# Kernel tuning notes

Measured on AMD Instinct MI355X. Metric: run time of the kernel, lower is better.

Reference implementation:

```python
import jax, jax.numpy as jnp
import numpy as np

B, N, C, H, REG = 1, 2309, 1024, 16, 5
D = C // H


def setup_inputs() -> dict:
    key = jax.random.key(0)
    k0, k1, k2, k3 = jax.random.split(key, 4)
    x = jax.random.normal(k0, (B, N, C), dtype=jnp.float32)
    g_info = jax.random.normal(k1, (12, 2, C), dtype=jnp.float32)
    W_qkv = jax.random.normal(k2, (C, 3 * C), dtype=jnp.float32) * 0.02
    W_proj = jax.random.normal(k3, (C, C), dtype=jnp.float32) * 0.02
    b_proj = jnp.zeros((C,), dtype=jnp.float32)
    return {"x": x, "g_info": g_info, "W_qkv": W_qkv, "W_proj": W_proj, "b_proj": b_proj}


def reference(x, g_info, W_qkv, W_proj, b_proj):
    Bx, Nx, Cx = x.shape
    scale = D ** -0.5
    # qkv projection (qkv_bias=False)
    qkv = (x @ W_qkv).reshape(Bx, Nx, 3, H, D)
    q, k, v = qkv[:, :, 0], qkv[:, :, 1], qkv[:, :, 2]  # [B,N,H,D]

    # grounding query vector from layer 0
    g_layer = g_info[0].reshape(-1, H, D)
    q_g = g_layer[0]  # [H,D]

    # cosine-similarity routing over non-register tokens
    q_pure = q[:, REG:]  # [B,M,H,D]
    q_n = q_pure / jnp.linalg.norm(q_pure, axis=-1, keepdims=True)
    qg_n = q_g / jnp.linalg.norm(q_g, axis=-1, keepdims=True)
    sim = (qg_n[None, None] * q_n).sum(-1).mean(-1)  # [B,M]
    sim = (sim - sim.min()) / (sim.max() - sim.min())  # global min-max normalize
    pos = sim > 0.9  # [B,M] boolean routing mask

    # Full logits computed once; group attention = masked softmax over the
    # group's key set (registers always included). This is mathematically
    # identical to the torch gather->attend->scatter, with static shapes.
    logits = jnp.einsum('bqhd,bkhd->bhqk', q * scale, k)  # [B,H,N,N]

    def masked_attn(tok_mask):
        key_mask = jnp.concatenate([jnp.ones((Bx, REG), bool), tok_mask], axis=1)  # [B,N]
        l = jnp.where(key_mask[:, None, None, :], logits, -jnp.inf)
        a = jax.nn.softmax(l, axis=-1)
        return jnp.einsum('bhqk,bkhd->bqhd', a, v)  # [B,N,H,D]

    x_pos = masked_attn(pos)
    x_neg = masked_attn(~pos)

    reg_out = (x_pos[:, :REG] + x_neg[:, :REG]) * 0.5
    tok_out = jnp.where(pos[:, :, None, None], x_pos[:, REG:], x_neg[:, REG:])
    out = jnp.concatenate([reg_out, tok_out], axis=1).reshape(Bx, Nx, Cx)
    return out @ W_proj + b_proj
```

## Files before the change

### kernel.cpp

```cpp
#include <hip/hip_runtime.h>
#include <math.h>

#define TOK 2309
#define CH 1024
#define NH 16
#define HD 64
#define NREG 5
#define NTOK (TOK - NREG)
#define NPADQ 2432
#define NPAD2 2432
#define NKT 38
#define HTILES 19
#define NQROW 2368
#define QSCL 0.1803368801f

typedef unsigned short ushort_t;
typedef unsigned char uchar_t;
typedef __attribute__((ext_vector_type(8))) short s8frag;
typedef __attribute__((ext_vector_type(4))) float f4frag;
typedef __attribute__((ext_vector_type(2))) long ll2;

__device__ __forceinline__ unsigned short f2bf(float x){
  union { float f; unsigned u; } v; v.f = x;
  unsigned r = v.u + 0x7FFF + ((v.u >> 16) & 1);
  return (unsigned short)(r >> 16);
}
__device__ __forceinline__ float bf2f(unsigned short u){
  union { unsigned u32; float f; } v; v.u32 = ((unsigned)u) << 16;
  return v.f;
}
__device__ __forceinline__ unsigned pack_bf16(float lo, float hi){
  union { float f; unsigned u; } a, b;
  a.f = lo; b.f = hi;
  return __builtin_amdgcn_perm(b.u + 0x8000u, a.u + 0x8000u, 0x07060302u);
}
__device__ __forceinline__ uchar_t f2fp8(float x){
  return (uchar_t)(__builtin_amdgcn_cvt_pk_fp8_f32(x, x, 0, false) & 0xff);
}
__device__ __forceinline__ void cp16(const void* g, void* l){
  __builtin_amdgcn_global_load_lds(
      (const __attribute__((address_space(1))) unsigned int*)g,
      (__attribute__((address_space(3))) unsigned int*)l, 16, 0, 0);
}

__global__ __launch_bounds__(256) void split_x_kernel(
    const float* __restrict__ X, ushort_t* __restrict__ Xbf)
{
  int row = blockIdx.x;
  int c4 = threadIdx.x * 4;
  ushort4 h4 = {0,0,0,0};
  if (row < TOK) {
    float4 v = *(const float4*)&X[(size_t)row*CH + c4];
    h4.x = f2bf(v.x); h4.y = f2bf(v.y); h4.z = f2bf(v.z); h4.w = f2bf(v.w);
  }
  *(ushort4*)&Xbf[(size_t)row*CH + c4] = h4;
}

__global__ __launch_bounds__(256) void pack_w_kernel(
    const float* __restrict__ Wqkv, const float* __restrict__ Wproj,
    ushort_t* __restrict__ WqkvT, ushort_t* __restrict__ WprojT)
{
  __shared__ float T[64][68];
  const int tid = threadIdx.x;
  int bx = blockIdx.x;
  const float* W; ushort_t* WT; int N;
  if (bx < 48) { W = Wqkv; WT = WqkvT; N = 3*CH; }
  else         { W = Wproj; WT = WprojT; N = CH; bx -= 48; }
  const int n0 = bx * 64;
  const int k0 = blockIdx.y * 64;
  const int lr = tid >> 4;
  const int lc = (tid & 15) * 4;
  #pragma unroll
  for (int s = 0; s < 4; s++) {
    float4 v = *(const float4*)&W[(size_t)(k0 + lr + s*16) * N + n0 + lc];
    *(float4*)&T[lr + s*16][lc] = v;
  }
  __syncthreads();
  const int nl = tid >> 2;
  const int kc = (tid & 3) * 16;
  ushort_t* dh = WT + (size_t)(n0 + nl) * CH + k0 + kc;
  #pragma unroll
  for (int g = 0; g < 4; g++) {
    ushort4 oh;
    oh.x = f2bf(T[kc+g*4+0][nl]); oh.y = f2bf(T[kc+g*4+1][nl]);
    oh.z = f2bf(T[kc+g*4+2][nl]); oh.w = f2bf(T[kc+g*4+3][nl]);
    *(ushort4*)&dh[g*4] = oh;
  }
}

__global__ __launch_bounds__(256) void ghat_kernel(
    const float* __restrict__ G, const float* __restrict__ Wqkv,
    float* __restrict__ U)
{
  const int tid = threadIdx.x;
  const int k = blockIdx.x * 16 + (tid >> 4);
  const int h = tid & 15;
  const float* g = G + h*64;
  float n2 = 0.f;
  #pragma unroll
  for (int d = 0; d < 64; d += 4) {
    float4 gv = *(const float4*)&g[d];
    n2 += gv.x*gv.x + gv.y*gv.y + gv.z*gv.z + gv.w*gv.w;
  }
  const float inv = 1.f / sqrtf(n2);
  const float* wr = Wqkv + (size_t)k*(3*CH) + h*64;
  float dot = 0.f;
  #pragma unroll
  for (int d = 0; d < 64; d += 4) {
    float4 wv = *(const float4*)&wr[d];
    float4 gv = *(const float4*)&g[d];
    dot += wv.x*gv.x + wv.y*gv.y + wv.z*gv.z + wv.w*gv.w;
  }
  U[h*CH + k] = dot * inv;
}

__global__ __launch_bounds__(256) void gemm_qkv_mfma(
    const ushort_t* __restrict__ Xbf, const ushort_t* __restrict__ WT,
    ushort_t* __restrict__ Qbf, uchar_t* __restrict__ Q8,
    uchar_t* __restrict__ K8, ushort_t* __restrict__ Vbf)
{
  __shared__ ushort_t LA[2][4096];
  __shared__ ushort_t LB[2][4096];
  const int tid = threadIdx.x;
  const int w = tid >> 6, lane = tid & 63;
  const int quad = lane >> 4, c16 = lane & 15;
  const int wm = w >> 1, wn = w & 1;
  const int nt = blockIdx.x, mt = blockIdx.y;
  const int n0 = nt * 128, m0 = mt * 128;

  const int srow = tid >> 2;
  const int g = (tid & 3) ^ ((tid >> 3) & 3);
  const size_t aoff = (size_t)(m0 + srow)*CH + g*8;
  const size_t boff = (size_t)(n0 + srow)*CH + g*8;
  const int lbase = (tid & 192) * 8;

  f4frag acc[4][4];
  #pragma unroll
  for (int mi = 0; mi < 4; mi++)
    #pragma unroll
    for (int nb = 0; nb < 4; nb++) acc[mi][nb] = (f4frag){0.f,0.f,0.f,0.f};

  const int soff = (quad ^ ((c16 >> 1) & 3)) * 8;
  int aro[4], bro[4];
  #pragma unroll
  for (int i = 0; i < 4; i++) {
    aro[i] = (wm*64 + i*16 + c16)*32 + soff;
    bro[i] = (wn*64 + i*16 + c16)*32 + soff;
  }

#define QKV_STAGE(KT, BUF) {                                                   \
    const int _k = (KT)*32;                                                    \
    cp16(Xbf + aoff + _k,                 &LA[BUF][lbase]);                    \
    cp16(Xbf + aoff + _k + (size_t)64*CH, &LA[BUF][2048 + lbase]);             \
    cp16(WT  + boff + _k,                 &LB[BUF][lbase]);                    \
    cp16(WT  + boff + _k + (size_t)64*CH, &LB[BUF][2048 + lbase]);             \
    }

  QKV_STAGE(0, 0);
  for (int kt = 0; kt < 32; kt++) {
    const int buf = kt & 1;
    __syncthreads();
    if (kt < 31) { QKV_STAGE(kt+1, buf^1); }
    s8frag a[4], b[4];
    #pragma unroll
    for (int i = 0; i < 4; i++) a[i] = *(const s8frag*)&LA[buf][aro[i]];
    #pragma unroll
    for (int i = 0; i < 4; i++) b[i] = *(const s8frag*)&LB[buf][bro[i]];
    #pragma unroll
    for (int mi = 0; mi < 4; mi++)
      #pragma unroll
      for (int nb = 0; nb < 4; nb++)
        acc[mi][nb] = __builtin_amdgcn_mfma_f32_16x16x32_bf16(a[mi], b[nb], acc[mi][nb], 0, 0, 0);
  }
#undef QKV_STAGE

  const int three = (nt >= 16) ? 2 : (nt >= 8) ? 1 : 0;
  #pragma unroll
  for (int mi = 0; mi < 4; mi++) {
    const int orow = m0 + wm*64 + mi*16 + quad*4;
    if (three == 0) {
      #pragma unroll
      for (int nb = 0; nb < 4; nb++) {
        const int col = n0 + wn*64 + nb*16 + c16;
        const int h = (col >> 6) & 15, d = col & 63;
        ushort_t* qb = Qbf + (size_t)h*NPADQ*64;
        uchar_t*  q8 = Q8 + (size_t)h*NPADQ*64;
        #pragma unroll
        for (int r = 0; r < 4; r++) {
          int row = orow + r;
          float v = (row < TOK) ? acc[mi][nb][r] : 0.f;
          qb[(size_t)row*64 + d] = f2bf(v);
          q8[(size_t)row*64 + d] = f2fp8(v);
        }
      }
    } else if (three == 1) {
      #pragma unroll
      for (int nb = 0; nb < 4; nb++) {
        const int col = n0 + wn*64 + nb*16 + c16;
        const int h = (col >> 6) & 15;
        const int quadK = ((nb & 1) * 2) + (c16 >> 3);
        const int byteoff = (nb >> 1) * 8 + (c16 & 7);
        uchar_t* base = K8 + (size_t)h*NKT*4096;
        #pragma unroll
        for (int r = 0; r < 4; r++) {
          int row = orow + r;
          float v = (row < TOK) ? acc[mi][nb][r] * QSCL : 0.f;
          int tile = row >> 6, b = (row >> 4) & 3, c16K = row & 15;
          base[(size_t)tile*4096 + b*1024 + (quadK*16 + c16K)*16 + byteoff] = f2fp8(v);
        }
      }
    } else {
      const int tile  = orow >> 6;
      const int jj    = orow & 63;
      const int c     = jj >> 5;
      const int t16   = (jj >> 4) & 1;
      const int quadA = (jj >> 2) & 3;
      #pragma unroll
      for (int nb = 0; nb < 4; nb++) {
        const int col = n0 + wn*64 + nb*16 + c16;
        const int h = (col >> 6) & 15, d = col & 63;
        const int dblk = d >> 4, c16A = d & 15;
        ushort_t* base = Vbf + (size_t)h*NKT*4096;
        ushort4 o;
        o.x = f2bf((orow+0 < TOK) ? acc[mi][nb][0] : 0.f);
        o.y = f2bf((orow+1 < TOK) ? acc[mi][nb][1] : 0.f);
        o.z = f2bf((orow+2 < TOK) ? acc[mi][nb][2] : 0.f);
        o.w = f2bf((orow+3 < TOK) ? acc[mi][nb][3] : 0.f);
        *(ushort4*)&base[(size_t)tile*4096 + dblk*1024 + c*512
                         + (quadA*16 + c16A)*8 + 4*t16] = o;
      }
    }
  }
}

__global__ __launch_bounds__(256) void sim_kernel(
    const float* __restrict__ X, const float* __restrict__ U,
    const ushort_t* __restrict__ Qbf, float* __restrict__ sim)
{
  const int gid = blockIdx.x*256 + threadIdx.x;
  const int it = gid >> 4;
  const int h  = gid & 15;
  const int row = NREG + it;
  const float* xr = X + (size_t)row*CH;
  const float* ur = U + h*CH;
  float num = 0.f;
  for (int k = 0; k < CH; k += 4) {
    float4 xv = *(const float4*)&xr[k];
    float4 uv = *(const float4*)&ur[k];
    num += xv.x*uv.x + xv.y*uv.y + xv.z*uv.z + xv.w*uv.w;
  }
  const ushort_t* qr = Qbf + ((size_t)h*NPADQ + row)*64;
  float n2 = 0.f;
  #pragma unroll
  for (int d = 0; d < 64; d += 4) {
    ushort4 a = *(const ushort4*)&qr[d];
    float q0 = bf2f(a.x), q1 = bf2f(a.y), q2 = bf2f(a.z), q3 = bf2f(a.w);
    n2 += q0*q0 + q1*q1 + q2*q2 + q3*q3;
  }
  float acc = num / sqrtf(n2);
  acc += __shfl_xor(acc, 1, 64);
  acc += __shfl_xor(acc, 2, 64);
  acc += __shfl_xor(acc, 4, 64);
  acc += __shfl_xor(acc, 8, 64);
  if (h == 0) sim[it] = acc * (1.0f/16.0f);
}

__global__ __launch_bounds__(256) void mask_kernel(
    const float* __restrict__ sim, int* __restrict__ cls,
    float* __restrict__ WP, float* __restrict__ WN)
{
  __shared__ float smn[256], smx[256];
  const int tid = threadIdx.x;
  float mn = 1e30f, mx = -1e30f;
  for (int i = tid; i < NTOK; i += 256) { float s = sim[i]; mn = fminf(mn, s); mx = fmaxf(mx, s); }
  smn[tid] = mn; smx[tid] = mx;
  __syncthreads();
  for (int off = 128; off > 0; off >>= 1) {
    if (tid < off) { smn[tid] = fminf(smn[tid], smn[tid+off]); smx[tid] = fmaxf(smx[tid], smx[tid+off]); }
    __syncthreads();
  }
  mn = smn[0]; mx = smx[0];
  float inv = 1.0f / (mx - mn);
  for (int j = tid; j < NPAD2; j += 256) {
    float wp = 0.f, wn = 0.f; int c = 0;
    if (j < NREG) { wp = 1.f; wn = 1.f; c = 2; }
    else if (j < TOK) {
      bool pos = ((sim[j-NREG] - mn) * inv) > 0.9f;
      c = pos ? 1 : 0;
      wp = pos ? 1.f : 0.f;
      wn = pos ? 0.f : 1.f;
    }
    WP[j] = wp; WN[j] = wn;
    if (j < TOK) cls[j] = c;
  }
}

__global__ __launch_bounds__(256) void attn_kernel(
    const uchar_t* __restrict__ Q8, const uchar_t* __restrict__ K8,
    const ushort_t* __restrict__ Vbf,
    const float* __restrict__ WP, const float* __restrict__ WN,
    ushort_t* __restrict__ POp, ushort_t* __restrict__ POn,
    float* __restrict__ Lp, float* __restrict__ Ln)
{
  __shared__ __align__(16) uchar_t smem[24576];
  uchar_t* Kst = smem;
  uchar_t* Vst = smem + 8192;
  const int tid = threadIdx.x;
  const int w = tid >> 6, lane = tid & 63;
  const int quad = lane >> 4, c16 = lane & 15;
  const int h = blockIdx.y;
  const int half = blockIdx.z;
  const int q0 = blockIdx.x * 64;

  const uchar_t* Qh = Q8 + (size_t)h * NPADQ * 64;
  const uchar_t* gk = K8 + ((size_t)h*NKT + half*HTILES)*4096 + tid*16;
  const uchar_t* gv = (const uchar_t*)Vbf + ((size_t)h*NKT + half*HTILES)*8192 + tid*16;
  const int lw = w * 1024;

  const uchar_t* qp = Qh + (size_t)(q0 + w*16 + c16)*64 + quad*8;
  const long qf0 = *(const long*)(qp);
  const long qf1 = *(const long*)(qp + 32);

  f4frag op[4], on[4];
  #pragma unroll
  for (int nb = 0; nb < 4; nb++) { op[nb] = (f4frag){0.f,0.f,0.f,0.f}; on[nb] = (f4frag){0.f,0.f,0.f,0.f}; }
  float lp = 0.f, ln = 0.f;

  cp16(gk, Kst + lw);
  cp16(gv, Vst + lw);
  cp16(gv + 4096, Vst + 4096 + lw);

  int pb = 0;
  for (int t = 0; t < HTILES; t++) {
    __syncthreads();
    if (t < HTILES-1) {
      cp16(gk + (size_t)(t+1)*4096, Kst + (pb^1)*4096 + lw);
      cp16(gv + (size_t)(t+1)*8192,        Vst + (pb^1)*8192 + lw);
      cp16(gv + (size_t)(t+1)*8192 + 4096, Vst + (pb^1)*8192 + 4096 + lw);
    }
    const int j0 = half*(HTILES*64) + t*64;
    f4frag st[4];
    #pragma unroll
    for (int b = 0; b < 4; b++) {
      ll2 kv = *(const ll2*)&Kst[pb*4096 + b*1024 + lane*16];
      f4frag z = (f4frag){0.f,0.f,0.f,0.f};
      z     = __builtin_amdgcn_mfma_f32_16x16x32_fp8_fp8(kv.x, qf0, z, 0, 0, 0);
      st[b] = __builtin_amdgcn_mfma_f32_16x16x32_fp8_fp8(kv.y, qf1, z, 0, 0, 0);
    }
    unsigned pu[4][2], nu[4][2];
    #pragma unroll
    for (int b = 0; b < 4; b++) {
      float4 wp4 = *(const float4*)&WP[j0 + b*16 + quad*4];
      float4 wn4 = *(const float4*)&WN[j0 + b*16 + quad*4];
      float p0 = __builtin_amdgcn_exp2f(st[b][0]);
      float p1 = __builtin_amdgcn_exp2f(st[b][1]);
      float p2 = __builtin_amdgcn_exp2f(st[b][2]);
      float p3 = __builtin_amdgcn_exp2f(st[b][3]);
      float a0 = p0*wp4.x, a1 = p1*wp4.y, a2 = p2*wp4.z, a3 = p3*wp4.w;
      float b0 = p0*wn4.x, b1 = p1*wn4.y, b2 = p2*wn4.z, b3 = p3*wn4.w;
      lp += (a0+a1)+(a2+a3);
      ln += (b0+b1)+(b2+b3);
      pu[b][0] = pack_bf16(a0, a1); pu[b][1] = pack_bf16(a2, a3);
      nu[b][0] = pack_bf16(b0, b1); nu[b][1] = pack_bf16(b2, b3);
    }
    union Frag { unsigned u[4]; s8frag v; };
    Frag fp0, fp1, fn0, fn1;
    fp0.u[0]=pu[0][0]; fp0.u[1]=pu[0][1]; fp0.u[2]=pu[1][0]; fp0.u[3]=pu[1][1];
    fp1.u[0]=pu[2][0]; fp1.u[1]=pu[2][1]; fp1.u[2]=pu[3][0]; fp1.u[3]=pu[3][1];
    fn0.u[0]=nu[0][0]; fn0.u[1]=nu[0][1]; fn0.u[2]=nu[1][0]; fn0.u[3]=nu[1][1];
    fn1.u[0]=nu[2][0]; fn1.u[1]=nu[2][1]; fn1.u[2]=nu[3][0]; fn1.u[3]=nu[3][1];
    #pragma unroll
    for (int nb = 0; nb < 4; nb++) {
      s8frag va = *(const s8frag*)&Vst[pb*8192 + nb*2048 + lane*16];
      s8frag vb = *(const s8frag*)&Vst[pb*8192 + nb*2048 + 1024 + lane*16];
      op[nb] = __builtin_amdgcn_mfma_f32_16x16x32_bf16(va, fp0.v, op[nb], 0, 0, 0);
      op[nb] = __builtin_amdgcn_mfma_f32_16x16x32_bf16(vb, fp1.v, op[nb], 0, 0, 0);
      on[nb] = __builtin_amdgcn_mfma_f32_16x16x32_bf16(va, fn0.v, on[nb], 0, 0, 0);
      on[nb] = __builtin_amdgcn_mfma_f32_16x16x32_bf16(vb, fn1.v, on[nb], 0, 0, 0);
    }
    pb ^= 1;
  }

  lp += __shfl_xor(lp, 16, 64); lp += __shfl_xor(lp, 32, 64);
  ln += __shfl_xor(ln, 16, 64); ln += __shfl_xor(ln, 32, 64);
  const int iq = q0 + w*16 + c16;
  if (quad == 0 && iq < TOK) {
    Lp[((size_t)half*NH + h)*NQROW + iq] = lp;
    Ln[((size_t)half*NH + h)*NQROW + iq] = ln;
  }
  if (iq < TOK) {
    const size_t base = (size_t)half*NQROW*CH + (size_t)iq*CH + h*HD;
    #pragma unroll
    for (int nb = 0; nb < 4; nb++) {
      uint2 po, no;
      po.x = pack_bf16(op[nb][0], op[nb][1]);
      po.y = pack_bf16(op[nb][2], op[nb][3]);
      no.x = pack_bf16(on[nb][0], on[nb][1]);
      no.y = pack_bf16(on[nb][2], on[nb][3]);
      *(uint2*)(POp + base + nb*16 + quad*4) = po;
      *(uint2*)(POn + base + nb*16 + quad*4) = no;
    }
  }
}

__global__ __launch_bounds__(256) void merge_kernel(
    const ushort_t* __restrict__ POp, const ushort_t* __restrict__ POn,
    const float* __restrict__ Lp, const float* __restrict__ Ln,
    const int* __restrict__ cls, ushort_t* __restrict__ AObf)
{
  const int row = blockIdx.x;
  const int c4 = threadIdx.x * 4;
  const int h = c4 >> 6;
  const size_t o0 = (size_t)row*CH + c4;
  const size_t o1 = (size_t)NQROW*CH + o0;
  ushort4 p0 = *(const ushort4*)(POp + o0);
  ushort4 p1 = *(const ushort4*)(POp + o1);
  ushort4 n0 = *(const ushort4*)(POn + o0);
  ushort4 n1 = *(const ushort4*)(POn + o1);
  const float lpt = Lp[(size_t)h*NQROW + row] + Lp[(size_t)(NH+h)*NQROW + row];
  const float lnt = Ln[(size_t)h*NQROW + row] + Ln[(size_t)(NH+h)*NQROW + row];
  const float ilp = 1.f / lpt, iln = 1.f / lnt;
  const int cq = cls[row];
  float vp[4], vn[4], o[4];
  vp[0] = (bf2f(p0.x)+bf2f(p1.x))*ilp; vn[0] = (bf2f(n0.x)+bf2f(n1.x))*iln;
  vp[1] = (bf2f(p0.y)+bf2f(p1.y))*ilp; vn[1] = (bf2f(n0.y)+bf2f(n1.y))*iln;
  vp[2] = (bf2f(p0.z)+bf2f(p1.z))*ilp; vn[2] = (bf2f(n0.z)+bf2f(n1.z))*iln;
  vp[3] = (bf2f(p0.w)+bf2f(p1.w))*ilp; vn[3] = (bf2f(n0.w)+bf2f(n1.w))*iln;
  if (row < NREG) {
    #pragma unroll
    for (int i = 0; i < 4; i++) o[i] = 0.5f*(vp[i]+vn[i]);
  } else if (cq == 1) {
    #pragma unroll
    for (int i = 0; i < 4; i++) o[i] = vp[i];
  } else {
    #pragma unroll
    for (int i = 0; i < 4; i++) o[i] = vn[i];
  }
  uint2 pk;
  pk.x = pack_bf16(o[0], o[1]);
  pk.y = pack_bf16(o[2], o[3]);
  *(uint2*)(AObf + (size_t)row*CH + c4) = pk;
}

__global__ __launch_bounds__(256) void gemm_proj_mfma(
    const ushort_t* __restrict__ A, const ushort_t* __restrict__ WT,
    const float* __restrict__ bp, float* __restrict__ out)
{
  __shared__ ushort_t LA[2][4096];
  __shared__ ushort_t LB[2][2048];
  const int tid = threadIdx.x;
  const int w = tid >> 6, lane = tid & 63;
  const int quad = lane >> 4, c16 = lane & 15;
  const int wm = w >> 1, wn = w & 1;
  const int nt = blockIdx.x, mt = blockIdx.y;
  const int n0 = nt * 64, m0 = mt * 128;

  const int srow = tid >> 2;
  const int g = (tid & 3) ^ ((tid >> 3) & 3);
  const size_t aoff = (size_t)(m0 + srow)*CH + g*8;
  const size_t boff = (size_t)(n0 + srow)*CH + g*8;
  const int lbase = (tid & 192) * 8;

  f4frag acc[4][2];
  #pragma unroll
  for (int mi = 0; mi < 4; mi++)
    #pragma unroll
    for (int nb = 0; nb < 2; nb++) acc[mi][nb] = (f4frag){0.f,0.f,0.f,0.f};

  const int soff = (quad ^ ((c16 >> 1) & 3)) * 8;
  int aro[4], bro[2];
  #pragma unroll
  for (int i = 0; i < 4; i++) aro[i] = (wm*64 + i*16 + c16)*32 + soff;
  #pragma unroll
  for (int i = 0; i < 2; i++) bro[i] = (wn*32 + i*16 + c16)*32 + soff;

#define PROJ_STAGE(KT, BUF) {                                                  \
    const int _k = (KT)*32;                                                    \
    cp16(A  + aoff + _k,                 &LA[BUF][lbase]);                     \
    cp16(A  + aoff + _k + (size_t)64*CH, &LA[BUF][2048 + lbase]);              \
    cp16(WT + boff + _k,                 &LB[BUF][lbase]);                     \
    }

  PROJ_STAGE(0, 0);
  for (int kt = 0; kt < 32; kt++) {
    const int buf = kt & 1;
    __syncthreads();
    if (kt < 31) { PROJ_STAGE(kt+1, buf^1); }
    s8frag a[4], b[2];
    #pragma unroll
    for (int i = 0; i < 4; i++) a[i] = *(const s8frag*)&LA[buf][aro[i]];
    #pragma unroll
    for (int i = 0; i < 2; i++) b[i] = *(const s8frag*)&LB[buf][bro[i]];
    #pragma unroll
    for (int mi = 0; mi < 4; mi++)
      #pragma unroll
      for (int nb = 0; nb < 2; nb++)
        acc[mi][nb] = __builtin_amdgcn_mfma_f32_16x16x32_bf16(a[mi], b[nb], acc[mi][nb], 0, 0, 0);
  }
#undef PROJ_STAGE

  #pragma unroll
  for (int mi = 0; mi < 4; mi++) {
    const int orow = m0 + wm*64 + mi*16 + quad*4;
    #pragma unroll
    for (int nb = 0; nb < 2; nb++) {
      const int col = n0 + wn*32 + nb*16 + c16;
      const float bias = bp[col];
      #pragma unroll
      for (int r = 0; r < 4; r++) {
        int row = orow + r;
        if (row < TOK) out[(size_t)row*CH + col] = acc[mi][nb][r] + bias;
      }
    }
  }
}

extern "C" void kernel_launch(void* const* d_in, const int* in_sizes, int n_in,
                              void* d_out, int out_size, void* d_ws, size_t ws_size,
                              hipStream_t stream) {
  const float* x      = (const float*)d_in[0];
  const float* g_info = (const float*)d_in[1];
  const float* W_qkv  = (const float*)d_in[2];
  const float* W_proj = (const float*)d_in[3];
  const float* b_proj = (const float*)d_in[4];
  float* out = (float*)d_out;

  float* ws = (float*)d_ws;
  float* SIM = ws;
  float* WP  = SIM + NTOK;
  float* WN  = WP + NPAD2;
  int*   CLS = (int*)(WN + NPAD2);
  float* LpB = (float*)(CLS + 2312);
  float* LnB = LpB + (size_t)2*NH*NQROW;
  float* U   = LnB + (size_t)2*NH*NQROW;
  ushort_t* Xbf    = (ushort_t*)(U + (size_t)NH*CH);
  ushort_t* WqkvT  = Xbf    + (size_t)NPADQ*CH;
  ushort_t* WprojT = WqkvT  + (size_t)3*CH*CH;
  ushort_t* Qbf    = WprojT + (size_t)CH*CH;
  ushort_t* AObf   = Qbf    + (size_t)NH*NPADQ*64;
  ushort_t* POp    = AObf   + (size_t)NPADQ*CH;
  ushort_t* POn    = POp    + (size_t)2*NQROW*CH;
  uchar_t*  Q8     = (uchar_t*)(POn + (size_t)2*NQROW*CH);
  uchar_t*  K8     = Q8 + (size_t)NH*NPADQ*64;
  ushort_t* Vbf    = (ushort_t*)(K8 + (size_t)NH*NKT*4096);

  split_x_kernel<<<dim3(NPADQ), 256, 0, stream>>>(x, Xbf);
  pack_w_kernel<<<dim3(64, 16), 256, 0, stream>>>(W_qkv, W_proj, WqkvT, WprojT);
  ghat_kernel<<<dim3(64), 256, 0, stream>>>(g_info, W_qkv, U);
  gemm_qkv_mfma<<<dim3(24, 19), 256, 0, stream>>>(Xbf, WqkvT, Qbf, Q8, K8, Vbf);
  sim_kernel<<<dim3(144), 256, 0, stream>>>(x, U, Qbf, SIM);
  mask_kernel<<<dim3(1), 256, 0, stream>>>(SIM, CLS, WP, WN);
  attn_kernel<<<dim3(37, NH, 2), 256, 0, stream>>>(Q8, K8, Vbf, WP, WN,
                                                   POp, POn, LpB, LnB);
  merge_kernel<<<dim3(TOK), 256, 0, stream>>>(POp, POn, LpB, LnB, CLS, AObf);
  gemm_proj_mfma<<<dim3(16, 19), 256, 0, stream>>>(AObf, WprojT, b_proj, out);
}
```

Baseline: 265.0 us.

## Fuse prep kernels into one launch and parallelize sim over tokens

Merges the x bf16 conversion, weight transpose/pack and grounding-vector projection into a single prep kernel dispatched by block index, removing two kernel launches. The sim kernel is restructured so each block handles one token: x is staged in LDS, the 1024-long dot product is split across 16 segments per head against a transposed U layout, and partial sums are reduced through shared memory. This is meant to replace the old 144-block launch, where each thread looped over all 1024 channels, with much more parallelism. The cost is more blocks and extra LDS traffic and syncs.

After: 232.2 us. 1.14x faster.

```diff
diff --git a/kernel.cpp b/kernel.cpp
--- a/kernel.cpp
+++ b/kernel.cpp
@@ -43,75 +43,76 @@
       (__attribute__((address_space(3))) unsigned int*)l, 16, 0, 0);
 }
 
-__global__ __launch_bounds__(256) void split_x_kernel(
-    const float* __restrict__ X, ushort_t* __restrict__ Xbf)
-{
-  int row = blockIdx.x;
-  int c4 = threadIdx.x * 4;
-  ushort4 h4 = {0,0,0,0};
-  if (row < TOK) {
-    float4 v = *(const float4*)&X[(size_t)row*CH + c4];
-    h4.x = f2bf(v.x); h4.y = f2bf(v.y); h4.z = f2bf(v.z); h4.w = f2bf(v.w);
-  }
-  *(ushort4*)&Xbf[(size_t)row*CH + c4] = h4;
-}
-
-__global__ __launch_bounds__(256) void pack_w_kernel(
-    const float* __restrict__ Wqkv, const float* __restrict__ Wproj,
-    ushort_t* __restrict__ WqkvT, ushort_t* __restrict__ WprojT)
-{
-  __shared__ float T[64][68];
+__global__ __launch_bounds__(256) void prep_kernel(
+    const float* __restrict__ X, const float* __restrict__ Wqkv,
+    const float* __restrict__ Wproj, const float* __restrict__ G,
+    ushort_t* __restrict__ Xbf, ushort_t* __restrict__ WqkvT,
+    ushort_t* __restrict__ WprojT, float* __restrict__ UT)
+{
   const int tid = threadIdx.x;
   int bx = blockIdx.x;
-  const float* W; ushort_t* WT; int N;
-  if (bx < 48) { W = Wqkv; WT = WqkvT; N = 3*CH; }
-  else         { W = Wproj; WT = WprojT; N = CH; bx -= 48; }
-  const int n0 = bx * 64;
-  const int k0 = blockIdx.y * 64;
-  const int lr = tid >> 4;
-  const int lc = (tid & 15) * 4;
-  #pragma unroll
-  for (int s = 0; s < 4; s++) {
-    float4 v = *(const float4*)&W[(size_t)(k0 + lr + s*16) * N + n0 + lc];
-    *(float4*)&T[lr + s*16][lc] = v;
-  }
-  __syncthreads();
-  const int nl = tid >> 2;
-  const int kc = (tid & 3) * 16;
-  ushort_t* dh = WT + (size_t)(n0 + nl) * CH + k0 + kc;
-  #pragma unroll
-  for (int g = 0; g < 4; g++) {
-    ushort4 oh;
-    oh.x = f2bf(T[kc+g*4+0][nl]); oh.y = f2bf(T[kc+g*4+1][nl]);
-    oh.z = f2bf(T[kc+g*4+2][nl]); oh.w = f2bf(T[kc+g*4+3][nl]);
-    *(ushort4*)&dh[g*4] = oh;
-  }
-}
-
-__global__ __launch_bounds__(256) void ghat_kernel(
-    const float* __restrict__ G, const float* __restrict__ Wqkv,
-    float* __restrict__ U)
-{
-  const int tid = threadIdx.x;
-  const int k = blockIdx.x * 16 + (tid >> 4);
-  const int h = tid & 15;
-  const float* g = G + h*64;
-  float n2 = 0.f;
-  #pragma unroll
-  for (int d = 0; d < 64; d += 4) {
-    float4 gv = *(const float4*)&g[d];
-    n2 += gv.x*gv.x + gv.y*gv.y + gv.z*gv.z + gv.w*gv.w;
-  }
-  const float inv = 1.f / sqrtf(n2);
-  const float* wr = Wqkv + (size_t)k*(3*CH) + h*64;
-  float dot = 0.f;
-  #pragma unroll
-  for (int d = 0; d < 64; d += 4) {
-    float4 wv = *(const float4*)&wr[d];
-    float4 gv = *(const float4*)&g[d];
-    dot += wv.x*gv.x + wv.y*gv.y + wv.z*gv.z + wv.w*gv.w;
-  }
-  U[h*CH + k] = dot * inv;
+  if (bx < NPADQ) {
+    const int row = bx;
+    const int c4 = tid * 4;
+    ushort4 h4 = {0,0,0,0};
+    if (row < TOK) {
+      float4 v = *(const float4*)&X[(size_t)row*CH + c4];
+      h4.x = f2bf(v.x); h4.y = f2bf(v.y); h4.z = f2bf(v.z); h4.w = f2bf(v.w);
+    }
+    *(ushort4*)&Xbf[(size_t)row*CH + c4] = h4;
+    return;
+  }
+  bx -= NPADQ;
+  if (bx < 1024) {
+    __shared__ float T[64][68];
+    int nb_i = bx & 63;
+    const int k0 = (bx >> 6) * 64;
+    const float* W; ushort_t* WT; int N;
+    if (nb_i < 48) { W = Wqkv; WT = WqkvT; N = 3*CH; }
+    else           { W = Wproj; WT = WprojT; N = CH; nb_i -= 48; }
+    const int n0 = nb_i * 64;
+    const int lr = tid >> 4;
+    const int lc = (tid & 15) * 4;
+    #pragma unroll
+    for (int s = 0; s < 4; s++) {
+      float4 v = *(const float4*)&W[(size_t)(k0 + lr + s*16) * N + n0 + lc];
+      *(float4*)&T[lr + s*16][lc] = v;
+    }
+    __syncthreads();
+    const int nl = tid >> 2;
+    const int kc = (tid & 3) * 16;
+    ushort_t* dh = WT + (size_t)(n0 + nl) * CH + k0 + kc;
+    #pragma unroll
+    for (int g = 0; g < 4; g++) {
+      ushort4 oh;
+      oh.x = f2bf(T[kc+g*4+0][nl]); oh.y = f2bf(T[kc+g*4+1][nl]);
+      oh.z = f2bf(T[kc+g*4+2][nl]); oh.w = f2bf(T[kc+g*4+3][nl]);
+      *(ushort4*)&dh[g*4] = oh;
+    }
+    return;
+  }
+  bx -= 1024;
+  {
+    const int k = bx * 16 + (tid >> 4);
+    const int h = tid & 15;
+    const float* g = G + h*64;
+    float n2 = 0.f;
+    #pragma unroll
+    for (int d = 0; d < 64; d += 4) {
+      float4 gv = *(const float4*)&g[d];
+      n2 += gv.x*gv.x + gv.y*gv.y + gv.z*gv.z + gv.w*gv.w;
+    }
+    const float inv = 1.f / sqrtf(n2);
+    const float* wr = Wqkv + (size_t)k*(3*CH) + h*64;
+    float dot = 0.f;
+    #pragma unroll
+    for (int d = 0; d < 64; d += 4) {
+      float4 wv = *(const float4*)&wr[d];
+      float4 gv = *(const float4*)&g[d];
+      dot += wv.x*gv.x + wv.y*gv.y + wv.z*gv.z + wv.w*gv.w;
+    }
+    UT[k*16 + h] = dot * inv;
+  }
 }
 
 __global__ __launch_bounds__(256) void gemm_qkv_mfma(
@@ -234,35 +235,39 @@
 }
 
 __global__ __launch_bounds__(256) void sim_kernel(
-    const float* __restrict__ X, const float* __restrict__ U,
+    const float* __restrict__ X, const float* __restrict__ UT,
     const ushort_t* __restrict__ Qbf, float* __restrict__ sim)
 {
-  const int gid = blockIdx.x*256 + threadIdx.x;
-  const int it = gid >> 4;
-  const int h  = gid & 15;
-  const int row = NREG + it;
-  const float* xr = X + (size_t)row*CH;
-  const float* ur = U + h*CH;
+  __shared__ float xs[1024];
+  __shared__ float pnum[16][17];
+  __shared__ float pn2[16][17];
+  const int tid = threadIdx.x;
+  const int row = NREG + blockIdx.x;
+  *(float4*)&xs[tid*4] = *(const float4*)&X[(size_t)row*CH + tid*4];
+  __syncthreads();
+  const int h = tid & 15, seg = tid >> 4;
+  const int k0 = seg * 64;
   float num = 0.f;
-  for (int k = 0; k < CH; k += 4) {
-    float4 xv = *(const float4*)&xr[k];
-    float4 uv = *(const float4*)&ur[k];
-    num += xv.x*uv.x + xv.y*uv.y + xv.z*uv.z + xv.w*uv.w;
-  }
-  const ushort_t* qr = Qbf + ((size_t)h*NPADQ + row)*64;
-  float n2 = 0.f;
-  #pragma unroll
-  for (int d = 0; d < 64; d += 4) {
-    ushort4 a = *(const ushort4*)&qr[d];
-    float q0 = bf2f(a.x), q1 = bf2f(a.y), q2 = bf2f(a.z), q3 = bf2f(a.w);
-    n2 += q0*q0 + q1*q1 + q2*q2 + q3*q3;
-  }
-  float acc = num / sqrtf(n2);
-  acc += __shfl_xor(acc, 1, 64);
-  acc += __shfl_xor(acc, 2, 64);
-  acc += __shfl_xor(acc, 4, 64);
-  acc += __shfl_xor(acc, 8, 64);
-  if (h == 0) sim[it] = acc * (1.0f/16.0f);
+  #pragma unroll
+  for (int j = 0; j < 64; j++)
+    num += xs[k0 + j] * UT[(k0 + j)*16 + h];
+  const ushort_t* qr = Qbf + ((size_t)h*NPADQ + row)*64 + seg*4;
+  ushort4 a = *(const ushort4*)qr;
+  float q0 = bf2f(a.x), q1 = bf2f(a.y), q2 = bf2f(a.z), q3 = bf2f(a.w);
+  pnum[seg][h] = num;
+  pn2[seg][h] = q0*q0 + q1*q1 + q2*q2 + q3*q3;
+  __syncthreads();
+  if (tid < 16) {
+    float nsum = 0.f, dsum = 0.f;
+    #pragma unroll
+    for (int s = 0; s < 16; s++) { nsum += pnum[s][tid]; dsum += pn2[s][tid]; }
+    float acc = nsum / sqrtf(dsum);
+    acc += __shfl_xor(acc, 1, 64);
+    acc += __shfl_xor(acc, 2, 64);
+    acc += __shfl_xor(acc, 4, 64);
+    acc += __shfl_xor(acc, 8, 64);
+    if (tid == 0) sim[blockIdx.x] = acc * (1.0f/16.0f);
+  }
 }
 
 __global__ __launch_bounds__(256) void mask_kernel(
@@ -532,8 +537,8 @@
   int*   CLS = (int*)(WN + NPAD2);
   float* LpB = (float*)(CLS + 2312);
   float* LnB = LpB + (size_t)2*NH*NQROW;
-  float* U   = LnB + (size_t)2*NH*NQROW;
-  ushort_t* Xbf    = (ushort_t*)(U + (size_t)NH*CH);
+  float* UT  = LnB + (size_t)2*NH*NQROW;
+  ushort_t* Xbf    = (ushort_t*)(UT + (size_t)CH*NH);
   ushort_t* WqkvT  = Xbf    + (size_t)NPADQ*CH;
   ushort_t* WprojT = WqkvT  + (size_t)3*CH*CH;
   ushort_t* Qbf    = WprojT + (size_t)CH*CH;
@@ -544,11 +549,10 @@
   uchar_t*  K8     = Q8 + (size_t)NH*NPADQ*64;
   ushort_t* Vbf    = (ushort_t*)(K8 + (size_t)NH*NKT*4096);
 
-  split_x_kernel<<<dim3(NPADQ), 256, 0, stream>>>(x, Xbf);
-  pack_w_kernel<<<dim3(64, 16), 256, 0, stream>>>(W_qkv, W_proj, WqkvT, WprojT);
-  ghat_kernel<<<dim3(64), 256, 0, stream>>>(g_info, W_qkv, U);
+  prep_kernel<<<dim3(NPADQ + 1024 + 64), 256, 0, stream>>>(
+      x, W_qkv, W_proj, g_info, Xbf, WqkvT, WprojT, UT);
   gemm_qkv_mfma<<<dim3(24, 19), 256, 0, stream>>>(Xbf, WqkvT, Qbf, Q8, K8, Vbf);
-  sim_kernel<<<dim3(144), 256, 0, stream>>>(x, U, Qbf, SIM);
+  sim_kernel<<<dim3(NTOK), 256, 0, stream>>>(x, UT, Qbf, SIM);
   mask_kernel<<<dim3(1), 256, 0, stream>>>(SIM, CLS, WP, WN);
   attn_kernel<<<dim3(37, NH, 2), 256, 0, stream>>>(Q8, K8, Vbf, WP, WN,
                                                    POp, POn, LpB, LnB);
```
